# Kernel optimization log

Measured on AMD Instinct MI355X. Metric: run time of the kernel, lower is better.

The kernel has to match this reference:

```python
import jax, jax.numpy as jnp
import numpy as np

K = 32
BN_EPS = 1e-5


def _fps(points, n_samples):
    # Sequential farthest point sampling; deterministic start at index 0
    # (torch version uses a random start; math otherwise identical).
    B, N, _ = points.shape

    def step(carry, _):
        dist_min, far = carry                                   # (B,N), (B,)
        c = jnp.take_along_axis(points, far[:, None, None].astype(jnp.int32) * jnp.ones((1, 1, 3), jnp.int32), axis=1)  # (B,1,3)
        d = jnp.sum((points - c) ** 2, axis=2)                  # (B,N)
        dist_min = jnp.minimum(dist_min, d)
        return (dist_min, jnp.argmax(dist_min, axis=1)), far

    init = (jnp.full((B, N), 1e10, points.dtype), jnp.zeros((B,), jnp.int64).astype(jnp.int32))
    _, cent = jax.lax.scan(step, init, None, length=n_samples)  # (n_samples, B)
    return cent.T                                               # (B, n_samples)


def _knn_idx(cntrds, pnts, k):
    # squared euclidean distance (same neighbor ordering as torch.cdist)
    d2 = (jnp.sum(cntrds ** 2, -1)[:, :, None]
          + jnp.sum(pnts ** 2, -1)[:, None, :]
          - 2.0 * jnp.einsum('bsc,bnc->bsn', cntrds, pnts))     # (B,ns,N)
    _, idx = jax.lax.top_k(-d2, k)                              # smallest-k
    return idx                                                  # (B,ns,k)


def _gather(x, idx):
    # x: (B,N,D), idx: (B,...) -> (B,...,D)
    return jax.vmap(lambda a, i: a[i])(x, idx)


def _conv1x1(x, w):
    # x: (B,Cin,ns,k), w: (Cout,Cin)
    return jnp.einsum('oc,bcnk->bonk', w, x)


def _bn_relu(x, g, b):
    # training-mode BatchNorm2d (biased variance over B,ns,k) + ReLU
    mean = jnp.mean(x, axis=(0, 2, 3), keepdims=True)
    var = jnp.var(x, axis=(0, 2, 3), keepdims=True)
    xh = (x - mean) * jax.lax.rsqrt(var + BN_EPS)
    return jax.nn.relu(xh * g[None, :, None, None] + b[None, :, None, None])


def setup_inputs() -> dict:
    key = jax.random.key(0)
    ks = jax.random.split(key, 16)
    B, N = 4, 4096
    s = 0.05
    return {
        'p': jax.random.normal(ks[0], (B, N, 3), jnp.float32),
        'f': jax.random.normal(ks[1], (B, 3, N), jnp.float32),
        'w1': jax.random.normal(ks[2], (256, 6), jnp.float32) * s,
        'w2': jax.random.normal(ks[3], (256, 256), jnp.float32) * s,
        'b2': jax.random.normal(ks[4], (256,), jnp.float32) * s,
        'g2': jnp.ones((256,), jnp.float32),
        'be2': jnp.zeros((256,), jnp.float32),
        'w3': jax.random.normal(ks[5], (512, 512), jnp.float32) * s,
        'g3': jnp.ones((512,), jnp.float32),
        'be3': jnp.zeros((512,), jnp.float32),
        'w4': jax.random.normal(ks[6], (256, 512), jnp.float32) * s,
        'g4': jnp.ones((256,), jnp.float32),
        'be4': jnp.zeros((256,), jnp.float32),
    }


def reference(p, f, w1, w2, b2, g2, be2, w3, g3, be3, w4, g4, be4):
    B, N, _ = p.shape
    ns = N // 4
    idx_c = _fps(p, ns)                                   # (B,ns)
    cntrd = _gather(p, idx_c)                             # (B,ns,3)
    feats = jnp.transpose(f, (0, 2, 1))                   # (B,N,3)
    knn = _knn_idx(cntrd, p, K)                           # (B,ns,K)
    dp = _gather(p, knn)                                  # (B,ns,K,3)
    fj = _gather(feats, knn)                              # (B,ns,K,3)
    x = jnp.transpose(jnp.concatenate([dp, fj], -1), (0, 3, 1, 2))  # (B,6,ns,K)
    # conv1: 6->256 (no bias), 256->256 (bias) + BN + ReLU
    x = _conv1x1(x, w1)
    x = _conv1x1(x, w2) + b2[None, :, None, None]
    x = _bn_relu(x, g2, be2)                              # (B,256,ns,K)
    xm = jnp.max(x, axis=-1, keepdims=True)
    x = jnp.concatenate([jnp.broadcast_to(xm, x.shape), x], axis=1)  # (B,512,ns,K)
    # conv2: 512->512 BN ReLU, 512->256 BN ReLU
    x = _bn_relu(_conv1x1(x, w3), g3, be3)
    x = _bn_relu(_conv1x1(x, w4), g4, be4)
    out_feat = jnp.max(x, axis=-1)                        # (B,256,ns)
    return cntrd, out_feat
```

## Files before the change

### kernel.cpp

```cpp
#include <hip/hip_runtime.h>
#include <hip/hip_bf16.h>

#define B_ 4
#define N_ 4096
#define NS_ 1024
#define KNN_ 32
#define NPOS_ 131072
#define BN_EPS_ 1e-5f

using bf16 = __hip_bfloat16;
typedef unsigned short us;
typedef __attribute__((ext_vector_type(8))) short short8;
typedef __attribute__((ext_vector_type(4))) float f32x4;
typedef unsigned long long ull;

__device__ __forceinline__ float bf2f(bf16 h){ return __bfloat162float(h); }
__device__ __forceinline__ us f2bfbits(float x){
    bf16 h = __float2bfloat16(x);
    return *reinterpret_cast<us*>(&h);
}
__device__ __forceinline__ float bits2f(us u){
    unsigned v = ((unsigned)u)<<16; return __uint_as_float(v);
}
__device__ __forceinline__ void unpack8(uint4 v, float* f){
    f[0]=__uint_as_float((v.x&0xFFFFu)<<16); f[1]=__uint_as_float(v.x&0xFFFF0000u);
    f[2]=__uint_as_float((v.y&0xFFFFu)<<16); f[3]=__uint_as_float(v.y&0xFFFF0000u);
    f[4]=__uint_as_float((v.z&0xFFFFu)<<16); f[5]=__uint_as_float(v.z&0xFFFF0000u);
    f[6]=__uint_as_float((v.w&0xFFFFu)<<16); f[7]=__uint_as_float(v.w&0xFFFF0000u);
}
__device__ __forceinline__ uint4 pack8(const float* f){
    uint4 v;
    v.x = (unsigned)f2bfbits(f[0]) | ((unsigned)f2bfbits(f[1])<<16);
    v.y = (unsigned)f2bfbits(f[2]) | ((unsigned)f2bfbits(f[3])<<16);
    v.z = (unsigned)f2bfbits(f[4]) | ((unsigned)f2bfbits(f[5])<<16);
    v.w = (unsigned)f2bfbits(f[6]) | ((unsigned)f2bfbits(f[7])<<16);
    return v;
}
__device__ __forceinline__ unsigned fmono(float v){
    unsigned u = __float_as_uint(v);
    return (u & 0x80000000u) ? ~u : (u | 0x80000000u);
}

template<int CTRL, int ROWM>
__device__ __forceinline__ float dppmaxf(float x){
    int xi = __float_as_int(x);
    int yi = __builtin_amdgcn_update_dpp(xi, xi, CTRL, ROWM, 0xF, false);
    return fmaxf(x, __int_as_float(yi));
}
template<int CTRL, int ROWM>
__device__ __forceinline__ float dppminf(float x){
    int xi = __float_as_int(x);
    int yi = __builtin_amdgcn_update_dpp(xi, xi, CTRL, ROWM, 0xF, false);
    return fminf(x, __int_as_float(yi));
}
__device__ __forceinline__ float wave_max_f32(float x){
    x = dppmaxf<0x111,0xF>(x);
    x = dppmaxf<0x112,0xF>(x);
    x = dppmaxf<0x114,0xF>(x);
    x = dppmaxf<0x118,0xF>(x);
    x = dppmaxf<0x142,0xA>(x);
    x = dppmaxf<0x143,0xC>(x);
    return __int_as_float(__builtin_amdgcn_readlane(__float_as_int(x), 63));
}
__device__ __forceinline__ float wave_min_f32(float x){
    x = dppminf<0x111,0xF>(x);
    x = dppminf<0x112,0xF>(x);
    x = dppminf<0x114,0xF>(x);
    x = dppminf<0x118,0xF>(x);
    x = dppminf<0x142,0xA>(x);
    x = dppminf<0x143,0xC>(x);
    return __int_as_float(__builtin_amdgcn_readlane(__float_as_int(x), 63));
}
__device__ __forceinline__ float rowsum16(float x){
    x += __int_as_float(__builtin_amdgcn_update_dpp(0, __float_as_int(x), 0x111, 0xF, 0xF, true));
    x += __int_as_float(__builtin_amdgcn_update_dpp(0, __float_as_int(x), 0x112, 0xF, 0xF, true));
    x += __int_as_float(__builtin_amdgcn_update_dpp(0, __float_as_int(x), 0x114, 0xF, 0xF, true));
    x += __int_as_float(__builtin_amdgcn_update_dpp(0, __float_as_int(x), 0x118, 0xF, 0xF, true));
    return x;
}
__device__ __forceinline__ float rowmax16(float x){
    x = dppmaxf<0x111,0xF>(x);
    x = dppmaxf<0x112,0xF>(x);
    x = dppmaxf<0x114,0xF>(x);
    x = dppmaxf<0x118,0xF>(x);
    return x;
}
__device__ __forceinline__ float rowmin16(float x){
    x = dppminf<0x111,0xF>(x);
    x = dppminf<0x112,0xF>(x);
    x = dppminf<0x114,0xF>(x);
    x = dppminf<0x118,0xF>(x);
    return x;
}
__device__ __forceinline__ float wave_sum_f32(float x){
    x = rowsum16(x);
    x += __int_as_float(__builtin_amdgcn_update_dpp(0, __float_as_int(x), 0x142, 0xA, 0xF, false));
    x += __int_as_float(__builtin_amdgcn_update_dpp(0, __float_as_int(x), 0x143, 0xC, 0xF, false));
    return __int_as_float(__builtin_amdgcn_readlane(__float_as_int(x), 63));
}
__device__ __forceinline__ float max16(const float* v){
    float a = fmaxf(fmaxf(fmaxf(v[0],v[1]),v[2]),v[3]);
    float b = fmaxf(fmaxf(fmaxf(v[4],v[5]),v[6]),v[7]);
    float c = fmaxf(fmaxf(fmaxf(v[8],v[9]),v[10]),v[11]);
    float d = fmaxf(fmaxf(fmaxf(v[12],v[13]),v[14]),v[15]);
    return fmaxf(fmaxf(a,b), fmaxf(c,d));
}
__device__ __forceinline__ float min16(const float* v){
    float a = fminf(fminf(fminf(v[0],v[1]),v[2]),v[3]);
    float b = fminf(fminf(fminf(v[4],v[5]),v[6]),v[7]);
    float c = fminf(fminf(fminf(v[8],v[9]),v[10]),v[11]);
    float d = fminf(fminf(fminf(v[12],v[13]),v[14]),v[15]);
    return fminf(fminf(a,b), fminf(c,d));
}

#define NSLOT 64

__global__ __launch_bounds__(256) void bn_coef(const float* __restrict__ part,
                                               const float* __restrict__ g,
                                               const float* __restrict__ be,
                                               int chbase, int C,
                                               float2* __restrict__ ab){
    int c = blockIdx.x*256 + threadIdx.x;
    if (c < C){
        const float* ps = part + (size_t)(chbase+c)*2*NSLOT;
        float s = 0.f, q = 0.f;
        #pragma unroll 8
        for (int i=0;i<NSLOT;i++){ s += ps[i]; q += ps[NSLOT+i]; }
        const float inv = 1.0f/(float)NPOS_;
        float mean = s*inv;
        float var  = q*inv - mean*mean;
        float a = g[c]*rsqrtf(var + BN_EPS_);
        ab[c] = make_float2(a, be[c] - mean*a);
    }
}

__global__ __launch_bounds__(256) void mega_kernel(const float* __restrict__ p,
                                                   const float* __restrict__ f,
                                                   float* __restrict__ cntrd,
                                                   float* __restrict__ part,
                                                   int* __restrict__ prog,
                                                   int* __restrict__ w26flag,
                                                   const float* __restrict__ w1,
                                                   const float* __restrict__ w2,
                                                   float* __restrict__ W26,
                                                   const float* __restrict__ b2,
                                                   const float* __restrict__ w3,
                                                   us* __restrict__ whi3,
                                                   const float* __restrict__ w4,
                                                   us* __restrict__ whi4,
                                                   bf16* __restrict__ z2,
                                                   us* __restrict__ mx2,
                                                   us* __restrict__ mn2){
    __shared__ float4 pxyz[N_];
    __shared__ ull warr[2][4];
    __shared__ int knnS[32];
    __shared__ float Ws[6][256];
    __shared__ float xs[6][32];
    __shared__ int ciS;
    const int bid = blockIdx.x;
    const int t = threadIdx.x;
    const int lane = t & 63;
    const int wave = t >> 6;

    if (bid < 4){
        __builtin_amdgcn_s_setprio(3);
        const int b = bid;
        const float* pb = p + (size_t)b*N_*3;
        float rx[16], ry[16], rz[16], dist[16];
        #pragma unroll
        for (int j=0;j<16;j++){
            int i = t*16+j;
            float x = pb[i*3+0];
            float y = pb[i*3+1];
            float z = pb[i*3+2];
            rx[j]=x; ry[j]=y; rz[j]=z;
            pxyz[i] = make_float4(x,y,z,0.f);
            dist[j]=1e10f;
        }
        __syncthreads();
        float4 c = pxyz[0];
        if (t==0){
            atomicExch(&prog[b*NS_], 1);
            cntrd[(size_t)(b*NS_)*3+0] = c.x;
            cntrd[(size_t)(b*NS_)*3+1] = c.y;
            cntrd[(size_t)(b*NS_)*3+2] = c.z;
        }
        for (int s=1; s<NS_; s++){
            #pragma unroll
            for (int j=0;j<16;j++){
                float dx = __fsub_rn(rx[j],c.x);
                float dy = __fsub_rn(ry[j],c.y);
                float dz = __fsub_rn(rz[j],c.z);
                float d  = __fadd_rn(__fadd_rn(__fmul_rn(dx,dx),__fmul_rn(dy,dy)),__fmul_rn(dz,dz));
                dist[j] = fminf(dist[j], d);
            }
            float lmax = max16(dist);
            float wmax = wave_max_f32(lmax);
            unsigned msk = 0;
            #pragma unroll
            for (int j=0;j<16;j++) msk |= (dist[j]==wmax) ? (1u<<j) : 0u;
            ull ball = __ballot(msk != 0);
            int srclane = (int)__builtin_ctzll(ball);
            unsigned lmsk = (unsigned)__builtin_amdgcn_readlane((int)msk, srclane);
            int widx = (wave*64 + srclane)*16 + (int)__builtin_ctz(lmsk);
            if (lane==0)
                warr[s&1][wave] = ((ull)__float_as_uint(wmax)<<32) | (0xFFFFFFFFu - (unsigned)widx);
            __syncthreads();
            ull g0 = warr[s&1][0], g1 = warr[s&1][1], g2 = warr[s&1][2], g3 = warr[s&1][3];
            ull ga = g0 > g1 ? g0 : g1;
            ull gb = g2 > g3 ? g2 : g3;
            ull g  = ga > gb ? ga : gb;
            int cur = (int)(0xFFFFFFFFu - (unsigned)(g & 0xFFFFFFFFull));
            c = pxyz[cur];
            if (t==0){
                atomicExch(&prog[b*NS_+s], cur+1);
                cntrd[(size_t)(b*NS_+s)*3+0] = c.x;
                cntrd[(size_t)(b*NS_+s)*3+1] = c.y;
                cntrd[(size_t)(b*NS_+s)*3+2] = c.z;
            }
        }
        return;
    }
    if (bid == 4){
        float acc[6] = {0,0,0,0,0,0};
        for (int k=0;k<256;k++){
            float w2v = w2[t*256+k];
            #pragma unroll
            for (int j=0;j<6;j++) acc[j] = fmaf(w2v, w1[k*6+j], acc[j]);
        }
        #pragma unroll
        for (int j=0;j<6;j++) W26[j*256+t] = acc[j];
        __syncthreads();
        if (t==0){ __threadfence(); atomicExch(w26flag, 1); }
        return;
    }
    if (bid < 1029){
        int i = (bid-5)*256 + t;
        whi3[i] = f2bfbits(w3[i]);
        return;
    }
    if (bid < 1541){
        int i = (bid-1029)*256 + t;
        whi4[i] = f2bfbits(w4[i]);
        return;
    }
    const int wid = bid - 1541;
    const int b = wid & 3;
    const int si = wid >> 2;
    const int sidx = b*NS_ + si;
    const float* pb = p + (size_t)b*N_*3;
    if (t == 0){
        int v;
        while ((v = atomicAdd(&prog[sidx], 0)) == 0) { __builtin_amdgcn_s_sleep(8); }
        ciS = v - 1;
    }
    __syncthreads();
    const int ci = ciS;
    float cx = pb[ci*3+0];
    float cy = pb[ci*3+1];
    float cz = pb[ci*3+2];
    float c2 = __fadd_rn(__fadd_rn(__fmul_rn(cx,cx),__fmul_rn(cy,cy)),__fmul_rn(cz,cz));
    float d2[16];
    #pragma unroll
    for (int j=0;j<16;j++){
        int i = t*16+j;
        float x = pb[i*3+0];
        float y = pb[i*3+1];
        float z = pb[i*3+2];
        float p2 = __fadd_rn(__fadd_rn(__fmul_rn(x,x),__fmul_rn(y,y)),__fmul_rn(z,z));
        float dot= __fadd_rn(__fadd_rn(__fmul_rn(cx,x),__fmul_rn(cy,y)),__fmul_rn(cz,z));
        d2[j] = __fsub_rn(__fadd_rn(c2,p2), __fmul_rn(2.0f,dot));
    }
    for (int it=0; it<KNN_; it++){
        float lmin = min16(d2);
        float wmin = wave_min_f32(lmin);
        unsigned msk = 0;
        #pragma unroll
        for (int j=0;j<16;j++) msk |= (d2[j]==wmin) ? (1u<<j) : 0u;
        ull ball = __ballot(msk != 0);
        int srclane = (int)__builtin_ctzll(ball);
        unsigned lmsk = (unsigned)__builtin_amdgcn_readlane((int)msk, srclane);
        int widx = (wave*64 + srclane)*16 + (int)__builtin_ctz(lmsk);
        if (lane==0)
            warr[it&1][wave] = ((ull)fmono(wmin)<<32) | (unsigned)widx;
        __syncthreads();
        ull g0 = warr[it&1][0], g1 = warr[it&1][1], g2 = warr[it&1][2], g3 = warr[it&1][3];
        ull ga = g0 < g1 ? g0 : g1;
        ull gb = g2 < g3 ? g2 : g3;
        ull g  = ga < gb ? ga : gb;
        int idx = (int)(g & 0xFFFFFFFFull);
        if ((idx>>4)==t) d2[idx & 15] = INFINITY;
        if (t==0) knnS[it] = idx;
    }
    if (t == 0){ while (atomicAdd(w26flag, 0) == 0) { __builtin_amdgcn_s_sleep(8); } __threadfence(); }
    __syncthreads();
    #pragma unroll
    for (int r=0;r<6;r++) Ws[r][t] = W26[r*256+t];
    if (t < 32){
        int i = knnS[t];
        const float* fb = f + (size_t)b*3*N_;
        xs[0][t] = pb[i*3+0];
        xs[1][t] = pb[i*3+1];
        xs[2][t] = pb[i*3+2];
        xs[3][t] = fb[0*N_+i];
        xs[4][t] = fb[1*N_+i];
        xs[5][t] = fb[2*N_+i];
    }
    __syncthreads();
    float w0=Ws[0][t], w1v=Ws[1][t], w2v=Ws[2][t], w3v=Ws[3][t], w4v=Ws[4][t], w5v=Ws[5][t];
    float bias = b2[t];
    bf16* zrow = z2 + (size_t)t*NPOS_ + (size_t)sidx*KNN_;
    float ssum = 0.f, sq = 0.f;
    float mxv = -3.4e38f, mnv = 3.4e38f;
    for (int k0=0;k0<32;k0+=8){
        float y[8];
        #pragma unroll
        for (int u=0;u<8;u++){
            int k = k0+u;
            float acc = bias;
            acc = fmaf(w0, xs[0][k], acc);
            acc = fmaf(w1v,xs[1][k], acc);
            acc = fmaf(w2v,xs[2][k], acc);
            acc = fmaf(w3v,xs[3][k], acc);
            acc = fmaf(w4v,xs[4][k], acc);
            acc = fmaf(w5v,xs[5][k], acc);
            float vr = bits2f(f2bfbits(acc));
            ssum += vr; sq = fmaf(vr, vr, sq);
            mxv = fmaxf(mxv, vr); mnv = fminf(mnv, vr);
            y[u] = acc;
        }
        *reinterpret_cast<uint4*>(zrow + k0) = pack8(y);
    }
    mx2[(size_t)t*4096 + sidx] = f2bfbits(mxv);
    mn2[(size_t)t*4096 + sidx] = f2bfbits(mnv);
    const int slot = wid & (NSLOT-1);
    atomicAdd(&part[(size_t)(t*2+0)*NSLOT + slot], ssum);
    atomicAdd(&part[(size_t)(t*2+1)*NSLOT + slot], sq);
}

__global__ __launch_bounds__(256) void xm_kernel(const us* __restrict__ mx2,
                                                 const us* __restrict__ mn2,
                                                 const float2* __restrict__ ab,
                                                 bf16* __restrict__ xm){
    int gid = blockIdx.x*256 + threadIdx.x;
    int c = gid >> 12;
    float2 s = ab[c];
    float x = (s.x >= 0.f) ? bits2f(mx2[gid]) : bits2f(mn2[gid]);
    float m = fmaxf(fmaf(x, s.x, s.y), 0.0f);
    xm[gid] = __float2bfloat16(m);
}

__global__ __launch_bounds__(256) void gemm128(const float* __restrict__ A, int lda, int aoff,
                                               const bf16* __restrict__ B,
                                               int M, int N, int K,
                                               float* __restrict__ Cf){
    __shared__ float As[16][128];
    __shared__ float Bs[16][128];
    const int tid = threadIdx.x;
    const int tx = tid & 15, ty = tid >> 4;
    const int m0 = blockIdx.y*128, n0 = blockIdx.x*128;
    float acc[8][8];
    #pragma unroll
    for (int i=0;i<8;i++)
        #pragma unroll
        for (int j=0;j<8;j++) acc[i][j]=0.f;
    const int arow = tid >> 1, akg = tid & 1;
    const int bkk = tid >> 4, bng = tid & 15;
    for (int k0=0;k0<K;k0+=16){
        const float* aptr = A + (size_t)(m0+arow)*lda + aoff + k0 + akg*8;
        float4 a0 = *reinterpret_cast<const float4*>(aptr);
        float4 a1 = *reinterpret_cast<const float4*>(aptr+4);
        As[akg*8+0][arow]=a0.x; As[akg*8+1][arow]=a0.y;
        As[akg*8+2][arow]=a0.z; As[akg*8+3][arow]=a0.w;
        As[akg*8+4][arow]=a1.x; As[akg*8+5][arow]=a1.y;
        As[akg*8+6][arow]=a1.z; As[akg*8+7][arow]=a1.w;
        uint4 bv = *reinterpret_cast<const uint4*>(B + (size_t)(k0+bkk)*N + n0 + bng*8);
        float bf[8]; unpack8(bv, bf);
        *reinterpret_cast<float4*>(&Bs[bkk][bng*8+0]) = make_float4(bf[0],bf[1],bf[2],bf[3]);
        *reinterpret_cast<float4*>(&Bs[bkk][bng*8+4]) = make_float4(bf[4],bf[5],bf[6],bf[7]);
        __syncthreads();
        #pragma unroll
        for (int kk=0;kk<16;kk++){
            float a[8], b[8];
            *reinterpret_cast<float4*>(&a[0]) = *reinterpret_cast<float4*>(&As[kk][ty*8+0]);
            *reinterpret_cast<float4*>(&a[4]) = *reinterpret_cast<float4*>(&As[kk][ty*8+4]);
            *reinterpret_cast<float4*>(&b[0]) = *reinterpret_cast<float4*>(&Bs[kk][tx*8+0]);
            *reinterpret_cast<float4*>(&b[4]) = *reinterpret_cast<float4*>(&Bs[kk][tx*8+4]);
            #pragma unroll
            for (int i=0;i<8;i++)
                #pragma unroll
                for (int j=0;j<8;j++)
                    acc[i][j] = fmaf(a[i], b[j], acc[i][j]);
        }
        __syncthreads();
    }
    const int n = n0 + tx*8;
    #pragma unroll
    for (int i=0;i<8;i++){
        int m = m0 + ty*8 + i;
        *reinterpret_cast<float4*>(Cf + (size_t)m*N + n + 0) = make_float4(acc[i][0],acc[i][1],acc[i][2],acc[i][3]);
        *reinterpret_cast<float4*>(Cf + (size_t)m*N + n + 4) = make_float4(acc[i][4],acc[i][5],acc[i][6],acc[i][7]);
    }
}

#define LDK 40
__global__ __launch_bounds__(256) void gemm_mfma(const us* __restrict__ Whi,
                                                 int ldw, int aoff,
                                                 const bf16* __restrict__ act, int K,
                                                 const float2* __restrict__ ab,
                                                 bf16* __restrict__ out,
                                                 const float* __restrict__ t3,
                                                 float* __restrict__ part, int chbase,
                                                 us* __restrict__ mxout,
                                                 us* __restrict__ mnout){
    __shared__ __align__(16) us AsH[128*LDK];
    __shared__ __align__(16) us Bs [128*LDK];
    __shared__ float t3s[128][4];
    const us* actu = reinterpret_cast<const us*>(act);
    const int t = threadIdx.x;
    const int m0 = blockIdx.x*128, n0 = blockIdx.y*128;
    const int wave = t>>6, lane = t&63;
    const int wm = wave>>1, wn = wave&1;
    const int q = lane>>4, col = lane&15;

    if (t3 && t < 128){
        const float* src = t3 + (size_t)(m0+t)*4096 + (n0>>5);
        t3s[t][0]=src[0]; t3s[t][1]=src[1]; t3s[t][2]=src[2]; t3s[t][3]=src[3];
    }

    f32x4 acc[4][4];
    #pragma unroll
    for (int i=0;i<4;i++)
        #pragma unroll
        for (int j=0;j<4;j++) acc[i][j] = (f32x4){0.f,0.f,0.f,0.f};

    const int ar = t>>1, ah = t&1;
    const int bn = t&127, bh = t>>7;

    for (int k0=0;k0<K;k0+=32){
        const us* sh = Whi + (size_t)(m0+ar)*ldw + aoff + k0 + ah*16;
        uint4 h0 = *reinterpret_cast<const uint4*>(sh);
        uint4 h1 = *reinterpret_cast<const uint4*>(sh+8);
        *reinterpret_cast<uint4*>(&AsH[ar*LDK + ah*16 + 0]) = h0;
        *reinterpret_cast<uint4*>(&AsH[ar*LDK + ah*16 + 8]) = h1;
        us bvals[16];
        #pragma unroll
        for (int j=0;j<16;j++){
            int k = k0 + bh*16 + j;
            float x = bits2f(actu[(size_t)k*NPOS_ + n0 + bn]);
            float2 s = ab[k];
            bvals[j] = f2bfbits(fmaxf(fmaf(x, s.x, s.y), 0.0f));
        }
        *reinterpret_cast<uint4*>(&Bs[bn*LDK + bh*16 + 0]) = *reinterpret_cast<uint4*>(&bvals[0]);
        *reinterpret_cast<uint4*>(&Bs[bn*LDK + bh*16 + 8]) = *reinterpret_cast<uint4*>(&bvals[8]);
        __syncthreads();
        short8 bf[4], afh[4];
        #pragma unroll
        for (int tn=0;tn<4;tn++)
            bf[tn] = *reinterpret_cast<const short8*>(&Bs[(wn*64+tn*16+col)*LDK + q*8]);
        #pragma unroll
        for (int tm=0;tm<4;tm++)
            afh[tm] = *reinterpret_cast<const short8*>(&AsH[(wm*64+tm*16+col)*LDK + q*8]);
        #pragma unroll
        for (int tm=0;tm<4;tm++)
            #pragma unroll
            for (int tn=0;tn<4;tn++)
                acc[tm][tn] = __builtin_amdgcn_mfma_f32_16x16x32_bf16(afh[tm], bf[tn], acc[tm][tn], 0, 0, 0);
        __syncthreads();
    }
    const int slot = (int)(blockIdx.y & (NSLOT-1));
    #pragma unroll
    for (int tm=0;tm<4;tm++){
        #pragma unroll
        for (int r=0;r<4;r++){
            int m_l = wm*64 + tm*16 + q*4 + r;
            float srow = 0.f, qrow = 0.f;
            float vr4[4];
            #pragma unroll
            for (int tn=0;tn<4;tn++){
                int n_l = wn*64 + tn*16 + col;
                float vv = acc[tm][tn][r];
                if (t3) vv += t3s[m_l][n_l>>5];
                us hb = f2bfbits(vv);
                if (!mxout)
                    reinterpret_cast<us*>(out)[(size_t)(m0+m_l)*NPOS_ + n0 + n_l] = hb;
                float vr = bits2f(hb);
                vr4[tn] = vr;
                srow += vr; qrow = fmaf(vr, vr, qrow);
            }
            srow = rowsum16(srow);
            qrow = rowsum16(qrow);
            if (col == 15){
                atomicAdd(&part[(size_t)((chbase + m0 + m_l)*2+0)*NSLOT + slot], srow);
                atomicAdd(&part[(size_t)((chbase + m0 + m_l)*2+1)*NSLOT + slot], qrow);
            }
            if (mxout){
                #pragma unroll
                for (int h=0;h<2;h++){
                    float mxl = fmaxf(vr4[2*h], vr4[2*h+1]);
                    float mnl = fminf(vr4[2*h], vr4[2*h+1]);
                    mxl = rowmax16(mxl);
                    mnl = rowmin16(mnl);
                    if (col == 15){
                        int bsi = (n0>>5) + wn*2 + h;
                        mxout[(size_t)(m0+m_l)*4096 + bsi] = f2bfbits(mxl);
                        mnout[(size_t)(m0+m_l)*4096 + bsi] = f2bfbits(mnl);
                    }
                }
            }
        }
    }
}

__global__ __launch_bounds__(256) void final_kernel(const us* __restrict__ mx4,
                                                    const us* __restrict__ mn4,
                                                    const float* __restrict__ part,
                                                    const float* __restrict__ g4,
                                                    const float* __restrict__ be4,
                                                    float* __restrict__ out){
    __shared__ float abS[2];
    const int t = threadIdx.x;
    const int c = (blockIdx.x >> 2) & 255;
    const int b = blockIdx.x >> 10;
    const int s = ((blockIdx.x & 3) << 8) | t;
    if (t < 64){
        float ss = part[(size_t)((768+c)*2+0)*NSLOT + t];
        float qq = part[(size_t)((768+c)*2+1)*NSLOT + t];
        ss = wave_sum_f32(ss);
        qq = wave_sum_f32(qq);
        if (t==0){
            const float inv = 1.0f/(float)NPOS_;
            float mean = ss*inv;
            float var  = qq*inv - mean*mean;
            float a = g4[c]*rsqrtf(var + BN_EPS_);
            abS[0] = a; abS[1] = be4[c] - mean*a;
        }
    }
    __syncthreads();
    const float a = abS[0], bb = abS[1];
    const int bsi = b*NS_ + s;
    float x = (a >= 0.f) ? bits2f(mx4[(size_t)c*4096 + bsi]) : bits2f(mn4[(size_t)c*4096 + bsi]);
    out[(size_t)(b*256 + c)*NS_ + s] = fmaxf(fmaf(x, a, bb), 0.0f);
}

extern "C" void kernel_launch(void* const* d_in, const int* in_sizes, int n_in,
                              void* d_out, int out_size, void* d_ws, size_t ws_size,
                              hipStream_t stream) {
    const float* p   = (const float*)d_in[0];
    const float* f   = (const float*)d_in[1];
    const float* w1  = (const float*)d_in[2];
    const float* w2  = (const float*)d_in[3];
    const float* b2  = (const float*)d_in[4];
    const float* g2  = (const float*)d_in[5];
    const float* be2 = (const float*)d_in[6];
    const float* w3  = (const float*)d_in[7];
    const float* g3  = (const float*)d_in[8];
    const float* be3 = (const float*)d_in[9];
    const float* w4  = (const float*)d_in[10];
    const float* g4  = (const float*)d_in[11];
    const float* be4 = (const float*)d_in[12];

    char* ws = (char*)d_ws;
    float*  W26  = (float*)(ws + 540672);
    float2* ab2  = (float2*)(ws + 555008);
    float2* ab3  = (float2*)(ws + 557056);
    us* whi3 = (us*)(ws + 561152);
    us* whi4 = (us*)(ws + 1609728);
    float*  t3   = (float*)(ws + 2134016);
    us*     mx2  = (us*)(ws + 2134016);
    us*     mn2  = (us*)(ws + 2134016 + 2097152);
    bf16*   z2   = (bf16*)(ws + 10522624);
    us*     mx4  = (us*)(ws + 10522624);
    us*     mn4  = (us*)(ws + 10522624 + 2097152);
    bf16*   xm   = (bf16*)(ws + 77631488);
    bf16*   z3   = (bf16*)(ws + 79728640);
    float*  part = (float*)(ws + 213946368);
    int*    prog = (int*)(ws + 214470656);
    int*    w26flag = (int*)(ws + 214487040);

    float* out_cntrd = (float*)d_out;
    float* out_feat  = (float*)d_out + (size_t)B_*NS_*3;

    hipMemsetAsync(ws + 213946368, 0, 540676, stream);
    mega_kernel<<<5637, 256, 0, stream>>>(p, f, out_cntrd, part, prog, w26flag,
                                          w1, w2, W26, b2,
                                          w3, whi3, w4, whi4, z2, mx2, mn2);
    bn_coef<<<1, 256, 0, stream>>>(part, g2, be2, 0, 256, ab2);
    xm_kernel<<<4096, 256, 0, stream>>>(mx2, mn2, ab2, xm);
    gemm128<<<dim3(32,4), 256, 0, stream>>>(w3, 512, 0, xm, 512, 4096, 256, t3);
    gemm_mfma<<<dim3(4,1024), 256, 0, stream>>>(whi3, 512, 256, z2, 256, ab2, z3, t3, part, 256,
                                                nullptr, nullptr);
    bn_coef<<<2, 256, 0, stream>>>(part, g3, be3, 256, 512, ab3);
    gemm_mfma<<<dim3(2,1024), 256, 0, stream>>>(whi4, 512, 0, z3, 512, ab3, nullptr, nullptr, part, 768,
                                                mx4, mn4);
    final_kernel<<<4096, 256, 0, stream>>>(mx4, mn4, part, g4, be4, out_feat);
}
```

Before: 1.049 ms.

## Pack max/min into one word, enlarge FPS LDS, drop setprio

Max and min bf16 values are now packed into a single 32-bit word, so each producer issues one store instead of two. The mega_kernel writes mxmn2 position-major for coalesced stores, and xm_kernel is rewritten to transpose it with 32 positions per thread and 16-byte stores. The pxyz shared array is padded, which raises LDS use and likely limits co-resident blocks next to the FPS blocks. The FPS wave priority boost is also removed. Together these change stores, occupancy and scheduling across several kernels.

```diff
diff --git a/kernel.cpp b/kernel.cpp
--- a/kernel.cpp
+++ b/kernel.cpp
@@ -134,6 +134,7 @@
     }
 }
 
+#define PXPAD 832
 __global__ __launch_bounds__(256) void mega_kernel(const float* __restrict__ p,
                                                    const float* __restrict__ f,
                                                    float* __restrict__ cntrd,
@@ -149,9 +150,8 @@
                                                    const float* __restrict__ w4,
                                                    us* __restrict__ whi4,
                                                    bf16* __restrict__ z2,
-                                                   us* __restrict__ mx2,
-                                                   us* __restrict__ mn2){
-    __shared__ float4 pxyz[N_];
+                                                   unsigned* __restrict__ mxmn2){
+    __shared__ float4 pxyz[N_ + PXPAD];
     __shared__ ull warr[2][4];
     __shared__ int knnS[32];
     __shared__ float Ws[6][256];
@@ -163,7 +163,6 @@
     const int wave = t >> 6;
 
     if (bid < 4){
-        __builtin_amdgcn_s_setprio(3);
         const int b = bid;
         const float* pb = p + (size_t)b*N_*3;
         float rx[16], ry[16], rz[16], dist[16];
@@ -331,23 +330,28 @@
         }
         *reinterpret_cast<uint4*>(zrow + k0) = pack8(y);
     }
-    mx2[(size_t)t*4096 + sidx] = f2bfbits(mxv);
-    mn2[(size_t)t*4096 + sidx] = f2bfbits(mnv);
+    mxmn2[(size_t)sidx*256 + t] = (unsigned)f2bfbits(mxv) | ((unsigned)f2bfbits(mnv)<<16);
     const int slot = wid & (NSLOT-1);
     atomicAdd(&part[(size_t)(t*2+0)*NSLOT + slot], ssum);
     atomicAdd(&part[(size_t)(t*2+1)*NSLOT + slot], sq);
 }
 
-__global__ __launch_bounds__(256) void xm_kernel(const us* __restrict__ mx2,
-                                                 const us* __restrict__ mn2,
+__global__ __launch_bounds__(256) void xm_kernel(const unsigned* __restrict__ mxmn2,
                                                  const float2* __restrict__ ab,
                                                  bf16* __restrict__ xm){
-    int gid = blockIdx.x*256 + threadIdx.x;
-    int c = gid >> 12;
-    float2 s = ab[c];
-    float x = (s.x >= 0.f) ? bits2f(mx2[gid]) : bits2f(mn2[gid]);
-    float m = fmaxf(fmaf(x, s.x, s.y), 0.0f);
-    xm[gid] = __float2bfloat16(m);
+    const int t = threadIdx.x;
+    const int bs0 = blockIdx.x * 32;
+    float2 s = ab[t];
+    us y[32];
+    #pragma unroll
+    for (int i=0;i<32;i++){
+        unsigned v = mxmn2[(size_t)(bs0+i)*256 + t];
+        float x = (s.x >= 0.f) ? bits2f((us)(v & 0xFFFFu)) : bits2f((us)(v >> 16));
+        y[i] = f2bfbits(fmaxf(fmaf(x, s.x, s.y), 0.0f));
+    }
+    uint4* dst = reinterpret_cast<uint4*>(reinterpret_cast<us*>(xm) + (size_t)t*4096 + bs0);
+    const uint4* src = reinterpret_cast<const uint4*>(y);
+    dst[0]=src[0]; dst[1]=src[1]; dst[2]=src[2]; dst[3]=src[3];
 }
 
 __global__ __launch_bounds__(256) void gemm128(const float* __restrict__ A, int lda, int aoff,
@@ -411,8 +415,7 @@
                                                  bf16* __restrict__ out,
                                                  const float* __restrict__ t3,
                                                  float* __restrict__ part, int chbase,
-                                                 us* __restrict__ mxout,
-                                                 us* __restrict__ mnout){
+                                                 unsigned* __restrict__ mxmnout){
     __shared__ __align__(16) us AsH[128*LDK];
     __shared__ __align__(16) us Bs [128*LDK];
     __shared__ float t3s[128][4];
@@ -482,7 +485,7 @@
                 float vv = acc[tm][tn][r];
                 if (t3) vv += t3s[m_l][n_l>>5];
                 us hb = f2bfbits(vv);
-                if (!mxout)
+                if (!mxmnout)
                     reinterpret_cast<us*>(out)[(size_t)(m0+m_l)*NPOS_ + n0 + n_l] = hb;
                 float vr = bits2f(hb);
                 vr4[tn] = vr;
@@ -494,26 +497,27 @@
                 atomicAdd(&part[(size_t)((chbase + m0 + m_l)*2+0)*NSLOT + slot], srow);
                 atomicAdd(&part[(size_t)((chbase + m0 + m_l)*2+1)*NSLOT + slot], qrow);
             }
-            if (mxout){
+            if (mxmnout){
+                unsigned pk[2];
                 #pragma unroll
                 for (int h=0;h<2;h++){
                     float mxl = fmaxf(vr4[2*h], vr4[2*h+1]);
                     float mnl = fminf(vr4[2*h], vr4[2*h+1]);
                     mxl = rowmax16(mxl);
                     mnl = rowmin16(mnl);
-                    if (col == 15){
-                        int bsi = (n0>>5) + wn*2 + h;
-                        mxout[(size_t)(m0+m_l)*4096 + bsi] = f2bfbits(mxl);
-                        mnout[(size_t)(m0+m_l)*4096 + bsi] = f2bfbits(mnl);
-                    }
+                    pk[h] = (unsigned)f2bfbits(mxl) | ((unsigned)f2bfbits(mnl)<<16);
+                }
+                if (col == 15){
+                    int bsi = (n0>>5) + wn*2;
+                    *reinterpret_cast<uint2*>(&mxmnout[(size_t)(m0+m_l)*4096 + bsi]) =
+                        make_uint2(pk[0], pk[1]);
                 }
             }
         }
     }
 }
 
-__global__ __launch_bounds__(256) void final_kernel(const us* __restrict__ mx4,
-                                                    const us* __restrict__ mn4,
+__global__ __launch_bounds__(256) void final_kernel(const unsigned* __restrict__ mxmn4,
                                                     const float* __restrict__ part,
                                                     const float* __restrict__ g4,
                                                     const float* __restrict__ be4,
@@ -539,7 +543,8 @@
     __syncthreads();
     const float a = abS[0], bb = abS[1];
     const int bsi = b*NS_ + s;
-    float x = (a >= 0.f) ? bits2f(mx4[(size_t)c*4096 + bsi]) : bits2f(mn4[(size_t)c*4096 + bsi]);
+    unsigned v = mxmn4[(size_t)c*4096 + bsi];
+    float x = (a >= 0.f) ? bits2f((us)(v & 0xFFFFu)) : bits2f((us)(v >> 16));
     out[(size_t)(b*256 + c)*NS_ + s] = fmaxf(fmaf(x, a, bb), 0.0f);
 }
 
@@ -561,22 +566,20 @@
     const float* be4 = (const float*)d_in[12];
 
     char* ws = (char*)d_ws;
-    float*  W26  = (float*)(ws + 540672);
-    float2* ab2  = (float2*)(ws + 555008);
-    float2* ab3  = (float2*)(ws + 557056);
-    us* whi3 = (us*)(ws + 561152);
-    us* whi4 = (us*)(ws + 1609728);
-    float*  t3   = (float*)(ws + 2134016);
-    us*     mx2  = (us*)(ws + 2134016);
-    us*     mn2  = (us*)(ws + 2134016 + 2097152);
-    bf16*   z2   = (bf16*)(ws + 10522624);
-    us*     mx4  = (us*)(ws + 10522624);
-    us*     mn4  = (us*)(ws + 10522624 + 2097152);
-    bf16*   xm   = (bf16*)(ws + 77631488);
-    bf16*   z3   = (bf16*)(ws + 79728640);
-    float*  part = (float*)(ws + 213946368);
-    int*    prog = (int*)(ws + 214470656);
-    int*    w26flag = (int*)(ws + 214487040);
+    float*    W26   = (float*)(ws + 540672);
+    float2*   ab2   = (float2*)(ws + 555008);
+    float2*   ab3   = (float2*)(ws + 557056);
+    us*       whi3  = (us*)(ws + 561152);
+    us*       whi4  = (us*)(ws + 1609728);
+    float*    t3    = (float*)(ws + 2134016);
+    unsigned* mxmn2 = (unsigned*)(ws + 2134016);
+    bf16*     z2    = (bf16*)(ws + 10522624);
+    unsigned* mxmn4 = (unsigned*)(ws + 10522624);
+    bf16*     xm    = (bf16*)(ws + 77631488);
+    bf16*     z3    = (bf16*)(ws + 79728640);
+    float*    part  = (float*)(ws + 213946368);
+    int*      prog  = (int*)(ws + 214470656);
+    int*      w26flag = (int*)(ws + 214487040);
 
     float* out_cntrd = (float*)d_out;
     float* out_feat  = (float*)d_out + (size_t)B_*NS_*3;
@@ -584,14 +587,14 @@
     hipMemsetAsync(ws + 213946368, 0, 540676, stream);
     mega_kernel<<<5637, 256, 0, stream>>>(p, f, out_cntrd, part, prog, w26flag,
                                           w1, w2, W26, b2,
-                                          w3, whi3, w4, whi4, z2, mx2, mn2);
+                                          w3, whi3, w4, whi4, z2, mxmn2);
     bn_coef<<<1, 256, 0, stream>>>(part, g2, be2, 0, 256, ab2);
-    xm_kernel<<<4096, 256, 0, stream>>>(mx2, mn2, ab2, xm);
+    xm_kernel<<<128, 256, 0, stream>>>(mxmn2, ab2, xm);
     gemm128<<<dim3(32,4), 256, 0, stream>>>(w3, 512, 0, xm, 512, 4096, 256, t3);
     gemm_mfma<<<dim3(4,1024), 256, 0, stream>>>(whi3, 512, 256, z2, 256, ab2, z3, t3, part, 256,
-                                                nullptr, nullptr);
+                                                nullptr);
     bn_coef<<<2, 256, 0, stream>>>(part, g3, be3, 256, 512, ab3);
     gemm_mfma<<<dim3(2,1024), 256, 0, stream>>>(whi4, 512, 0, z3, 512, ab3, nullptr, nullptr, part, 768,
-                                                mx4, mn4);
-    final_kernel<<<4096, 256, 0, stream>>>(mx4, mn4, part, g4, be4, out_feat);
-}
+                                                mxmn4);
+    final_kernel<<<4096, 256, 0, stream>>>(mxmn4, part, g4, be4, out_feat);
+}
```

After: 1.066 ms. About the same (+1.6%).
